# Optimization experiments

Hardware: AMD Instinct MI355X
Metric: run time of the kernel (lower is better)

Reference implementation:

```python
import jax, jax.numpy as jnp
import numpy as np

D_MODEL = 1024
NUM_HEADS = 16
HEAD_DIM = D_MODEL // NUM_HEADS


def setup_inputs() -> dict:
    key = jax.random.key(0)
    kx, kq, kk, kv, ko = jax.random.split(key, 5)
    B, S = 2, 2048
    scale = 1.0 / np.sqrt(D_MODEL)
    return {
        "x": jax.random.normal(kx, (B, S, D_MODEL), dtype=jnp.float32),
        "W_q": jax.random.normal(kq, (D_MODEL, D_MODEL), dtype=jnp.float32) * scale,
        "W_k": jax.random.normal(kk, (D_MODEL, D_MODEL), dtype=jnp.float32) * scale,
        "W_v": jax.random.normal(kv, (D_MODEL, D_MODEL), dtype=jnp.float32) * scale,
        "W_o": jax.random.normal(ko, (D_MODEL, D_MODEL), dtype=jnp.float32) * scale,
        "causal": 1,
    }


def _attn(x, W_q, W_k, W_v, W_o, causal):
    B, S, D = x.shape
    H, Hd = NUM_HEADS, HEAD_DIM
    # projections: nn.Linear applies x @ W.T
    q = (x @ W_q.T).reshape(B, S, H, Hd)
    k = (x @ W_k.T).reshape(B, S, H, Hd)
    v = (x @ W_v.T).reshape(B, S, H, Hd)
    # scores: [B, H, S, S]
    scores = jnp.einsum("bqhd,bkhd->bhqk", q, k) / np.sqrt(Hd)
    if causal:
        mask = jnp.triu(jnp.ones((S, S), dtype=bool), k=1)
        scores = jnp.where(mask, -jnp.inf, scores)
    attn = jax.nn.softmax(scores, axis=-1)
    out = jnp.einsum("bhqk,bkhd->bqhd", attn, v).reshape(B, S, D)
    return out @ W_o.T


def reference(x, W_q, W_k, W_v, W_o, causal):
    return _attn(x, W_q, W_k, W_v, W_o, causal)
```

## Files before the change

### kernel.cpp

```cpp
#include <hip/hip_runtime.h>

typedef __attribute__((ext_vector_type(8))) short bf16x8;
typedef __attribute__((ext_vector_type(4))) float f32x4;
typedef __attribute__((ext_vector_type(4))) unsigned short u16x4;

#define MFMA16(a, b, c) __builtin_amdgcn_mfma_f32_16x16x32_bf16((a), (b), (c), 0, 0, 0)

static constexpr int D_MODEL = 1024;
static constexpr int SEQ = 2048;
static constexpr int NH = 16;
static constexpr int HD = 64;
static constexpr int LDA = 40;
static constexpr int MST = 136;
static constexpr float NEG_BIG = -1.0e30f;

__device__ __forceinline__ unsigned short f2bf(float f) {
  union { float f; unsigned int u; } v; v.f = f;
  unsigned int r = v.u + 0x7fffu + ((v.u >> 16) & 1u);
  return (unsigned short)(r >> 16);
}

__device__ __forceinline__ unsigned int cvtpk_bf16(float a, float b) {
  unsigned int r;
  asm("v_cvt_pk_bf16_f32 %0, %1, %2" : "=v"(r) : "v"(a), "v"(b));
  return r;
}

__device__ __forceinline__ bf16x8 ld8(const void* p, size_t eidx, int bf) {
  if (bf) return *(const bf16x8*)((const unsigned short*)p + eidx);
  const float* f = (const float*)p + eidx;
  f32x4 lo = *(const f32x4*)f;
  f32x4 hi = *(const f32x4*)(f + 4);
  bf16x8 r;
  r[0] = (short)f2bf(lo[0]); r[1] = (short)f2bf(lo[1]);
  r[2] = (short)f2bf(lo[2]); r[3] = (short)f2bf(lo[3]);
  r[4] = (short)f2bf(hi[0]); r[5] = (short)f2bf(hi[1]);
  r[6] = (short)f2bf(hi[2]); r[7] = (short)f2bf(hi[3]);
  return r;
}

__device__ __forceinline__ void async16(const unsigned short* g, unsigned short* l) {
  __builtin_amdgcn_global_load_lds(
      (const __attribute__((address_space(1))) void*)g,
      (__attribute__((address_space(3))) void*)l, 16, 0, 0);
}

__global__ __launch_bounds__(64) void detect_kernel(
    const unsigned short* __restrict__ xs, int* __restrict__ flag) {
  int lane = threadIdx.x;
  unsigned short s = xs[2 * lane];
  int e = (s >> 7) & 0xFF;
  bool hit = (e >= 117 && e <= 129);
  unsigned long long m = __ballot(hit);
  if (lane == 0) { flag[0] = (__popcll(m) >= 32) ? 1 : 0; flag[1] = 1; }
}

__global__ __launch_bounds__(256) void convert_kernel(
    const void* __restrict__ X,
    const void* __restrict__ W0, const void* __restrict__ W1,
    const void* __restrict__ W2, const void* __restrict__ W3,
    const int* __restrict__ flag,
    unsigned short* __restrict__ Xb, unsigned short* __restrict__ Wb)
{
  const int bf = *flag;
  const int ty = blockIdx.y;
  const void* src; unsigned short* dst; size_t n;
  if (ty == 0) { src = X; dst = Xb; n = (size_t)2 * SEQ * D_MODEL; }
  else {
    src = (ty == 1) ? W0 : (ty == 2) ? W1 : (ty == 3) ? W2 : W3;
    dst = Wb + (size_t)(ty - 1) * D_MODEL * D_MODEL;
    n = (size_t)D_MODEL * D_MODEL;
  }
  size_t i = ((size_t)blockIdx.x * 256 + threadIdx.x) * 8;
  if (i >= n) return;
  *(bf16x8*)(dst + i) = ld8(src, i, bf);
}

__device__ __forceinline__ void gemm_fast_core(
    const unsigned short* __restrict__ A, const unsigned short* __restrict__ B,
    int tm, int tn, unsigned short* smem, f32x4 acc[4][4])
{
  const int t = threadIdx.x;
  const int lane = t & 63;
  const int w = t >> 6;
  const int wm = (w >> 1) * 64, wn = (w & 1) * 64;
  const int quad = lane >> 4, l16 = lane & 15;
  const int srow = lane >> 3;
  const int scol = ((lane & 7) ^ srow) * 8;
  const int xa = l16 & 7;

#pragma unroll
  for (int mi = 0; mi < 4; ++mi)
#pragma unroll
    for (int ni = 0; ni < 4; ++ni)
      acc[mi][ni] = (f32x4){0.f, 0.f, 0.f, 0.f};

#pragma unroll
  for (int j = 0; j < 4; ++j) {
    const int row = w * 32 + j * 8;
    async16(A + (size_t)(tm + row + srow) * D_MODEL + scol, smem + row * 64);
    async16(B + (size_t)(tn + row + srow) * D_MODEL + scol,
            smem + 8192 + row * 64);
  }

  for (int kt = 0; kt < 16; ++kt) {
    const int co = (kt & 1) << 14;
    asm volatile("s_waitcnt vmcnt(0)" ::: "memory");
    __syncthreads();
    if (kt < 15) {
      const int no = ((kt & 1) ^ 1) << 14;
      const int k0 = (kt + 1) * 64;
#pragma unroll
      for (int j = 0; j < 4; ++j) {
        const int row = w * 32 + j * 8;
        async16(A + (size_t)(tm + row + srow) * D_MODEL + k0 + scol,
                smem + no + row * 64);
        async16(B + (size_t)(tn + row + srow) * D_MODEL + k0 + scol,
                smem + no + 8192 + row * 64);
      }
    }
    bf16x8 af[2][4], bfv[2][4];
#pragma unroll
    for (int ks = 0; ks < 2; ++ks) {
#pragma unroll
      for (int mi = 0; mi < 4; ++mi)
        af[ks][mi] = *(const bf16x8*)(smem + co + (wm + mi * 16 + l16) * 64 +
                                      ((ks * 4 + quad) ^ xa) * 8);
#pragma unroll
      for (int ni = 0; ni < 4; ++ni)
        bfv[ks][ni] = *(const bf16x8*)(smem + co + 8192 +
                                       (wn + ni * 16 + l16) * 64 +
                                       ((ks * 4 + quad) ^ xa) * 8);
    }
    __builtin_amdgcn_s_setprio(1);
#pragma unroll
    for (int ks = 0; ks < 2; ++ks)
#pragma unroll
      for (int mi = 0; mi < 4; ++mi)
#pragma unroll
        for (int ni = 0; ni < 4; ++ni)
          acc[mi][ni] = MFMA16(af[ks][mi], bfv[ks][ni], acc[mi][ni]);
    __builtin_amdgcn_s_setprio(0);
  }
}

__global__ __launch_bounds__(256) void qkv_fast_kernel(
    const unsigned short* __restrict__ X,
    const unsigned short* __restrict__ Wb,
    unsigned short* __restrict__ qd,
    unsigned short* __restrict__ kws,
    unsigned short* __restrict__ vws)
{
  __shared__ __align__(16) unsigned short smem[4 * 128 * 64];
  const int bid = blockIdx.x;
  const int xcd = bid & 7, s0 = bid >> 3;
  const int tmg = xcd >> 2, tng = xcd & 3;
  const int tm_local = s0 / 6, zt = s0 % 6;
  const int z = zt >> 1, tn_local = zt & 1;
  const int tm = (tmg * 16 + tm_local) * 128;
  const int tn = (tng * 2 + tn_local) * 128;
  const unsigned short* W = Wb + (size_t)z * D_MODEL * D_MODEL;
  f32x4 acc[4][4];
  gemm_fast_core(X, W, tm, tn, smem, acc);

  const int t = threadIdx.x;
  const int lane = t & 63, w = t >> 6;
  const int wm = (w >> 1) * 64, wn = (w & 1) * 64;
  const int quad = lane >> 4, l16 = lane & 15;

  if (z == 2) {
    const int b = tm >> 11;
    const int sb = tm & 2047;
#pragma unroll
    for (int ph = 0; ph < 2; ++ph) {
      __syncthreads();
      if ((w & 1) == ph) {
#pragma unroll
        for (int mi = 0; mi < 4; ++mi)
#pragma unroll
          for (int ni = 0; ni < 4; ++ni)
#pragma unroll
            for (int r = 0; r < 4; ++r) {
              int m_local = wm + mi * 16 + quad * 4 + r;
              int n_sub = ni * 16 + l16;
              smem[n_sub * MST + m_local] = f2bf(acc[mi][ni][r]);
            }
      }
      __syncthreads();
      const int row = t >> 2, c0 = (t & 3) * 32;
      const int n_g = tn + ph * 64 + row;
      const int h = n_g >> 6, d = n_g & 63;
      unsigned short* dst = vws + (((size_t)b * NH + h) * HD + d) * SEQ + sb + c0;
#pragma unroll
      for (int cc = 0; cc < 4; ++cc)
        *(bf16x8*)(dst + cc * 8) = *(const bf16x8*)(smem + row * MST + c0 + cc * 8);
    }
    return;
  }
#pragma unroll
  for (int mi = 0; mi < 4; ++mi)
#pragma unroll
    for (int ni = 0; ni < 4; ++ni)
#pragma unroll
      for (int r = 0; r < 4; ++r) {
        int m = tm + wm + mi * 16 + quad * 4 + r;
        int n = tn + wn + ni * 16 + l16;
        unsigned short bv = f2bf(acc[mi][ni][r]);
        if (z == 0) {
          qd[(size_t)m * D_MODEL + n] = bv;
        } else {
          int b = m >> 11, sg = m & 2047;
          int h = n >> 6, d = n & 63;
          kws[(((size_t)b * NH + h) * SEQ + sg) * HD + d] = bv;
        }
      }
}

__global__ __launch_bounds__(256) void oproj_fast_kernel(
    const unsigned short* __restrict__ AW,
    const unsigned short* __restrict__ Wo,
    float* __restrict__ tmp)
{
  __shared__ __align__(16) unsigned short smem[4 * 128 * 64];
  const int bid = blockIdx.x;
  const int xcd = bid & 7, s0 = bid >> 3;
  const int tmg = xcd >> 2, tng = xcd & 3;
  const int tm = (tmg * 16 + (s0 >> 1)) * 128;
  const int tn = (tng * 2 + (s0 & 1)) * 128;
  f32x4 acc[4][4];
  gemm_fast_core(AW, Wo, tm, tn, smem, acc);

  const int t = threadIdx.x;
  const int lane = t & 63, w = t >> 6;
  const int wm = (w >> 1) * 64, wn = (w & 1) * 64;
  const int quad = lane >> 4, l16 = lane & 15;
#pragma unroll
  for (int mi = 0; mi < 4; ++mi)
#pragma unroll
    for (int ni = 0; ni < 4; ++ni)
#pragma unroll
      for (int r = 0; r < 4; ++r) {
        int m = tm + wm + mi * 16 + quad * 4 + r;
        int n = tn + wn + ni * 16 + l16;
        tmp[(size_t)m * D_MODEL + n] = acc[mi][ni][r];
      }
}

__device__ __forceinline__ void gemm_tile_128x128(
    const void* __restrict__ A, const void* __restrict__ B, int bf,
    int tm, int tn, unsigned short* As, unsigned short* Bs, f32x4 acc[4][4])
{
  const int t = threadIdx.x;
  const int lane = t & 63;
  const int w = t >> 6;
  const int wm = (w >> 1) * 64, wn = (w & 1) * 64;
  const int quad = lane >> 4, l16 = lane & 15;
  const int r0 = t >> 2, kc = (t & 3) * 8;
  const int r1 = r0 + 64;

#pragma unroll
  for (int mi = 0; mi < 4; ++mi)
#pragma unroll
    for (int ni = 0; ni < 4; ++ni)
      acc[mi][ni] = (f32x4){0.f, 0.f, 0.f, 0.f};

  for (int k0 = 0; k0 < D_MODEL; k0 += 32) {
    bf16x8 a0 = ld8(A, (size_t)(tm + r0) * D_MODEL + k0 + kc, bf);
    bf16x8 a1 = ld8(A, (size_t)(tm + r1) * D_MODEL + k0 + kc, bf);
    bf16x8 b0 = ld8(B, (size_t)(tn + r0) * D_MODEL + k0 + kc, bf);
    bf16x8 b1 = ld8(B, (size_t)(tn + r1) * D_MODEL + k0 + kc, bf);
    __syncthreads();
    *(bf16x8*)(As + r0 * LDA + kc) = a0;
    *(bf16x8*)(As + r1 * LDA + kc) = a1;
    *(bf16x8*)(Bs + r0 * LDA + kc) = b0;
    *(bf16x8*)(Bs + r1 * LDA + kc) = b1;
    __syncthreads();
    bf16x8 af[4], bfv[4];
#pragma unroll
    for (int mi = 0; mi < 4; ++mi)
      af[mi] = *(const bf16x8*)(As + (wm + mi * 16 + l16) * LDA + quad * 8);
#pragma unroll
    for (int ni = 0; ni < 4; ++ni)
      bfv[ni] = *(const bf16x8*)(Bs + (wn + ni * 16 + l16) * LDA + quad * 8);
#pragma unroll
    for (int mi = 0; mi < 4; ++mi)
#pragma unroll
      for (int ni = 0; ni < 4; ++ni)
        acc[mi][ni] = MFMA16(af[mi], bfv[ni], acc[mi][ni]);
  }
}

__global__ __launch_bounds__(256) void qkv_kernel(
    const void* __restrict__ X,
    const void* __restrict__ Wq,
    const void* __restrict__ Wk,
    const void* __restrict__ Wv,
    const int* __restrict__ flag,
    unsigned short* __restrict__ qd,
    unsigned short* __restrict__ kws,
    unsigned short* __restrict__ vws)
{
  __shared__ __align__(16) unsigned short As[128 * LDA];
  __shared__ __align__(16) unsigned short Bs[128 * LDA];
  const int bf = *flag;
  const int z = blockIdx.z;
  const void* W = (z == 0) ? Wq : ((z == 1) ? Wk : Wv);
  const int tm = blockIdx.y * 128, tn = blockIdx.x * 128;
  f32x4 acc[4][4];
  gemm_tile_128x128(X, W, bf, tm, tn, As, Bs, acc);

  const int t = threadIdx.x;
  const int lane = t & 63, w = t >> 6;
  const int wm = (w >> 1) * 64, wn = (w & 1) * 64;
  const int quad = lane >> 4, l16 = lane & 15;
#pragma unroll
  for (int mi = 0; mi < 4; ++mi)
#pragma unroll
    for (int ni = 0; ni < 4; ++ni)
#pragma unroll
      for (int r = 0; r < 4; ++r) {
        int m = tm + wm + mi * 16 + quad * 4 + r;
        int n = tn + wn + ni * 16 + l16;
        unsigned short bv = f2bf(acc[mi][ni][r]);
        if (z == 0) {
          qd[(size_t)m * D_MODEL + n] = bv;
        } else {
          int b = m >> 11, s = m & 2047;
          int h = n >> 6, d = n & 63;
          if (z == 1) kws[(((size_t)b * NH + h) * SEQ + s) * HD + d] = bv;
          else        vws[(((size_t)b * NH + h) * HD + d) * SEQ + s] = bv;
        }
      }
}

__global__ __launch_bounds__(256) void oproj_kernel(
    const unsigned short* __restrict__ AW,
    const void* __restrict__ Wo,
    const int* __restrict__ flag,
    float* __restrict__ tmp)
{
  __shared__ __align__(16) unsigned short As[128 * LDA];
  __shared__ __align__(16) unsigned short Bs[128 * LDA];
  const int bf = *flag;
  const int t = threadIdx.x;
  const int lane = t & 63;
  const int w = t >> 6;
  const int wm = (w >> 1) * 64, wn = (w & 1) * 64;
  const int quad = lane >> 4, l16 = lane & 15;
  const int r0 = t >> 2, kc = (t & 3) * 8;
  const int r1 = r0 + 64;
  const int tm = blockIdx.y * 128, tn = blockIdx.x * 128;
  f32x4 acc[4][4];
#pragma unroll
  for (int mi = 0; mi < 4; ++mi)
#pragma unroll
    for (int ni = 0; ni < 4; ++ni)
      acc[mi][ni] = (f32x4){0.f, 0.f, 0.f, 0.f};

  for (int k0 = 0; k0 < D_MODEL; k0 += 32) {
    bf16x8 a0 = *(const bf16x8*)(AW + (size_t)(tm + r0) * D_MODEL + k0 + kc);
    bf16x8 a1 = *(const bf16x8*)(AW + (size_t)(tm + r1) * D_MODEL + k0 + kc);
    bf16x8 b0 = ld8(Wo, (size_t)(tn + r0) * D_MODEL + k0 + kc, bf);
    bf16x8 b1 = ld8(Wo, (size_t)(tn + r1) * D_MODEL + k0 + kc, bf);
    __syncthreads();
    *(bf16x8*)(As + r0 * LDA + kc) = a0;
    *(bf16x8*)(As + r1 * LDA + kc) = a1;
    *(bf16x8*)(Bs + r0 * LDA + kc) = b0;
    *(bf16x8*)(Bs + r1 * LDA + kc) = b1;
    __syncthreads();
    bf16x8 af[4], bfv[4];
#pragma unroll
    for (int mi = 0; mi < 4; ++mi)
      af[mi] = *(const bf16x8*)(As + (wm + mi * 16 + l16) * LDA + quad * 8);
#pragma unroll
    for (int ni = 0; ni < 4; ++ni)
      bfv[ni] = *(const bf16x8*)(Bs + (wn + ni * 16 + l16) * LDA + quad * 8);
#pragma unroll
    for (int mi = 0; mi < 4; ++mi)
#pragma unroll
      for (int ni = 0; ni < 4; ++ni)
        acc[mi][ni] = MFMA16(af[mi], bfv[ni], acc[mi][ni]);
  }
#pragma unroll
  for (int mi = 0; mi < 4; ++mi)
#pragma unroll
    for (int ni = 0; ni < 4; ++ni)
#pragma unroll
      for (int r = 0; r < 4; ++r) {
        int m = tm + wm + mi * 16 + quad * 4 + r;
        int n = tn + wn + ni * 16 + l16;
        tmp[(size_t)m * D_MODEL + n] = acc[mi][ni][r];
      }
}

__global__ __launch_bounds__(128) void attn_kernel(
    unsigned short* __restrict__ Qd,
    const unsigned short* __restrict__ Kb,
    const unsigned short* __restrict__ Vt,
    const int* __restrict__ causal_p)
{
  __shared__ __align__(16) unsigned short Ks[2][64 * 64];
  __shared__ __align__(16) unsigned short Vs[2][64 * 64];
  const int bid = blockIdx.x;
  const int xcd = bid & 7, slot = bid >> 3;
  const int q = slot >> 5;
  const int r = slot & 31;
  const int gg = (q & 1) ? (31 - r) : r;
  const int bh = xcd * 4 + q;
  const int b = bh >> 4, h = bh & 15;
  const int t = threadIdx.x, lane = t & 63, w = t >> 6;
  const int quad = lane >> 4, l16 = lane & 15;
  const int causal = *causal_p;
  unsigned short* qh = Qd + (size_t)b * SEQ * D_MODEL + h * HD;
  const unsigned short* kh = Kb + ((size_t)b * NH + h) * SEQ * HD;
  const unsigned short* vh = Vt + ((size_t)b * NH + h) * HD * SEQ;
  const float Cs = 0.125f * 1.4426950408889634f;
  const int srow = lane >> 3;
  const int gcol = ((lane & 7) ^ srow) * 8;
  const int xa = l16 & 7;
  const int ktend = causal ? (gg + 1) : (SEQ / 64);

  int kvp[4];
#pragma unroll
  for (int j2 = 0; j2 < 4; ++j2) {
    const int rp = w * 32 + j2 * 8 + srow;
    kvp[j2] = ((rp >> 4) & 1) * 32 + ((rp >> 2) & 3) * 8 + ((rp >> 5) & 1) * 4 + (rp & 3);
  }

  int q0[2];
  bf16x8 aq[2][2];
#pragma unroll
  for (int s = 0; s < 2; ++s) {
    q0[s] = gg * 64 + w * 32 + s * 16;
#pragma unroll
    for (int ch = 0; ch < 2; ++ch)
      aq[s][ch] = *(const bf16x8*)(qh + (size_t)(q0[s] + l16) * D_MODEL +
                                   ch * 32 + quad * 8);
  }

  f32x4 oaccT[2][4];
#pragma unroll
  for (int s = 0; s < 2; ++s)
#pragma unroll
    for (int db = 0; db < 4; ++db) oaccT[s][db] = (f32x4){0.f, 0.f, 0.f, 0.f};
  float lsum[2] = {0.f, 0.f};

#pragma unroll
  for (int j2 = 0; j2 < 4; ++j2) {
    const int row = w * 32 + j2 * 8;
    async16(kh + (size_t)kvp[j2] * HD + gcol, &Ks[0][row * 64]);
    async16(vh + (size_t)(row + srow) * SEQ + gcol, &Vs[0][row * 64]);
  }

  for (int kt = 0; kt < ktend; ++kt) {
    const int cur = kt & 1;
    asm volatile("s_waitcnt vmcnt(0)" ::: "memory");
    __syncthreads();
    if (kt + 1 < ktend) {
      const int nxt = cur ^ 1;
#pragma unroll
      for (int j2 = 0; j2 < 4; ++j2) {
        const int row = w * 32 + j2 * 8;
        async16(kh + (size_t)((kt + 1) * 64 + kvp[j2]) * HD + gcol,
                &Ks[nxt][row * 64]);
        async16(vh + (size_t)(row + srow) * SEQ + (kt + 1) * 64 + gcol,
                &Vs[nxt][row * 64]);
      }
    }

    bf16x8 kfr[4][2], vfr[4][2];
#pragma unroll
    for (int cb = 0; cb < 4; ++cb)
#pragma unroll
      for (int hf = 0; hf < 2; ++hf) {
        kfr[cb][hf] = *(const bf16x8*)(&Ks[cur][(cb * 16 + l16) * 64 +
                                                ((hf * 4 + quad) ^ xa) * 8]);
        vfr[cb][hf] = *(const bf16x8*)(&Vs[cur][(cb * 16 + l16) * 64 +
                                                ((hf * 4 + quad) ^ xa) * 8]);
      }
#pragma unroll
    for (int s = 0; s < 2; ++s) {
      f32x4 sc[4];
      __builtin_amdgcn_s_setprio(1);
#pragma unroll
      for (int cb = 0; cb < 4; ++cb) {
        sc[cb] = (f32x4){0.f, 0.f, 0.f, 0.f};
        sc[cb] = MFMA16(kfr[cb][0], aq[s][0], sc[cb]);
        sc[cb] = MFMA16(kfr[cb][1], aq[s][1], sc[cb]);
      }
      __builtin_amdgcn_s_setprio(0);
      if (causal && kt == gg) {
        int qq = q0[s] + l16;
#pragma unroll
        for (int cb = 0; cb < 4; ++cb)
#pragma unroll
          for (int rr = 0; rr < 4; ++rr)
            if (kt * 64 + (cb & 1) * 32 + quad * 8 + (cb >> 1) * 4 + rr > qq)
              sc[cb][rr] = NEG_BIG;
      }
      float ls = 0.f;
#pragma unroll
      for (int cb = 0; cb < 4; ++cb)
#pragma unroll
        for (int rr = 0; rr < 4; ++rr) {
          float p = __builtin_amdgcn_exp2f(sc[cb][rr] * Cs);
          ls += p;
          sc[cb][rr] = p;
        }
      lsum[s] += ls;
      bf16x8 bp[2];
#pragma unroll
      for (int hf = 0; hf < 2; ++hf) {
        union { unsigned int w4[4]; bf16x8 v; } u;
        u.w4[0] = cvtpk_bf16(sc[hf][0], sc[hf][1]);
        u.w4[1] = cvtpk_bf16(sc[hf][2], sc[hf][3]);
        u.w4[2] = cvtpk_bf16(sc[2 + hf][0], sc[2 + hf][1]);
        u.w4[3] = cvtpk_bf16(sc[2 + hf][2], sc[2 + hf][3]);
        bp[hf] = u.v;
      }
      __builtin_amdgcn_s_setprio(1);
#pragma unroll
      for (int db = 0; db < 4; ++db) {
        oaccT[s][db] = MFMA16(vfr[db][0], bp[0], oaccT[s][db]);
        oaccT[s][db] = MFMA16(vfr[db][1], bp[1], oaccT[s][db]);
      }
      __builtin_amdgcn_s_setprio(0);
    }
  }
#pragma unroll
  for (int s = 0; s < 2; ++s) {
    float l = lsum[s];
    l += __shfl_xor(l, 16, 64);
    l += __shfl_xor(l, 32, 64);
    float inv = 1.0f / l;
#pragma unroll
    for (int db = 0; db < 4; ++db) {
      u16x4 o;
#pragma unroll
      for (int rr = 0; rr < 4; ++rr) o[rr] = f2bf(oaccT[s][db][rr] * inv);
      *(u16x4*)(qh + (size_t)(q0[s] + l16) * D_MODEL + db * 16 + quad * 4) = o;
    }
  }
}

__global__ __launch_bounds__(256) void final_kernel(
    const float* __restrict__ tmp, void* __restrict__ out,
    const int* __restrict__ flag)
{
  const int bf = *flag;
  size_t i = ((size_t)blockIdx.x * 256 + threadIdx.x) * 8;
  f32x4 lo = *(const f32x4*)(tmp + i);
  f32x4 hi = *(const f32x4*)(tmp + i + 4);
  if (bf) {
    bf16x8 r;
    r[0] = (short)f2bf(lo[0]); r[1] = (short)f2bf(lo[1]);
    r[2] = (short)f2bf(lo[2]); r[3] = (short)f2bf(lo[3]);
    r[4] = (short)f2bf(hi[0]); r[5] = (short)f2bf(hi[1]);
    r[6] = (short)f2bf(hi[2]); r[7] = (short)f2bf(hi[3]);
    *(bf16x8*)((unsigned short*)out + i) = r;
  } else {
    *(f32x4*)((float*)out + i) = lo;
    *(f32x4*)((float*)out + i + 4) = hi;
  }
}

extern "C" void kernel_launch(void* const* d_in, const int* in_sizes, int n_in,
                              void* d_out, int out_size, void* d_ws, size_t ws_size,
                              hipStream_t stream) {
  const void* X  = d_in[0];
  const void* Wq = d_in[1];
  const void* Wk = d_in[2];
  const void* Wv = d_in[3];
  const void* Wo = d_in[4];
  const int* causal = (const int*)d_in[5];

  const size_t NE = (size_t)2 * SEQ * D_MODEL;
  const size_t WE = (size_t)D_MODEL * D_MODEL;
  int* flag0 = (int*)d_ws;
  int* flag1 = flag0 + 1;
  unsigned short* kws = (unsigned short*)((char*)d_ws + 64);
  unsigned short* vws = kws + NE;
  float* tmp = (float*)kws;
  unsigned short* Wb = vws + NE;
  unsigned short* qd = (unsigned short*)d_out;
  unsigned short* Xb = qd + NE;

  const bool big = ws_size >= (size_t)64 + 24ull * 1024 * 1024;

  hipLaunchKernelGGL(detect_kernel, dim3(1), dim3(64), 0, stream,
                     (const unsigned short*)X, flag0);
  if (big) {
    hipLaunchKernelGGL(convert_kernel, dim3(2048, 5), dim3(256), 0, stream,
                       X, Wq, Wk, Wv, Wo, flag0, Xb, Wb);
    hipLaunchKernelGGL(qkv_fast_kernel, dim3(768), dim3(256), 0, stream,
                       Xb, Wb, qd, kws, vws);
    hipLaunchKernelGGL(attn_kernel, dim3(1024), dim3(128), 0, stream,
                       qd, kws, vws, causal);
    hipLaunchKernelGGL(oproj_fast_kernel, dim3(256), dim3(256), 0, stream,
                       qd, Wb + 3 * WE, tmp);
  } else {
    hipLaunchKernelGGL(qkv_kernel, dim3(8, 32, 3), dim3(256), 0, stream,
                       X, Wq, Wk, Wv, flag0, qd, kws, vws);
    hipLaunchKernelGGL(attn_kernel, dim3(1024), dim3(128), 0, stream,
                       qd, kws, vws, causal);
    hipLaunchKernelGGL(oproj_kernel, dim3(8, 32), dim3(256), 0, stream,
                       qd, Wo, flag0, tmp);
  }
  hipLaunchKernelGGL(final_kernel, dim3(2048), dim3(256), 0, stream,
                     tmp, d_out, flag0);
}
```

Measured before the change: 202.1 us.

## Pair complementary causal query tiles per attention block with triple-buffered KV

Measured after the change: 200.1 us. About the same (-1.0%).

```diff
diff --git a/kernel.cpp b/kernel.cpp
--- a/kernel.cpp
+++ b/kernel.cpp
@@ -393,24 +393,91 @@
       }
 }
 
-__global__ __launch_bounds__(128) void attn_kernel(
+__device__ __forceinline__ void attn_item(
+    const unsigned short* __restrict__ Ksb, const unsigned short* __restrict__ Vsb,
+    const bf16x8 (&aq)[2][2], f32x4 (&oaccT)[2][4], float (&lsum)[2],
+    int kt, int diag, int q0base, int l16, int quad, int xa, float Cs)
+{
+  bf16x8 kfr[4][2], vfr[4][2];
+#pragma unroll
+  for (int cb = 0; cb < 4; ++cb)
+#pragma unroll
+    for (int hf = 0; hf < 2; ++hf) {
+      kfr[cb][hf] = *(const bf16x8*)(Ksb + (cb * 16 + l16) * 64 +
+                                     ((hf * 4 + quad) ^ xa) * 8);
+      vfr[cb][hf] = *(const bf16x8*)(Vsb + (cb * 16 + l16) * 64 +
+                                     ((hf * 4 + quad) ^ xa) * 8);
+    }
+#pragma unroll
+  for (int s = 0; s < 2; ++s) {
+    f32x4 sc[4];
+    __builtin_amdgcn_s_setprio(1);
+#pragma unroll
+    for (int cb = 0; cb < 4; ++cb) {
+      sc[cb] = (f32x4){0.f, 0.f, 0.f, 0.f};
+      sc[cb] = MFMA16(kfr[cb][0], aq[s][0], sc[cb]);
+      sc[cb] = MFMA16(kfr[cb][1], aq[s][1], sc[cb]);
+    }
+    __builtin_amdgcn_s_setprio(0);
+    if (diag) {
+      int qq = q0base + s * 16 + l16;
+#pragma unroll
+      for (int cb = 0; cb < 4; ++cb)
+#pragma unroll
+        for (int rr = 0; rr < 4; ++rr)
+          if (kt * 64 + (cb & 1) * 32 + quad * 8 + (cb >> 1) * 4 + rr > qq)
+            sc[cb][rr] = NEG_BIG;
+    }
+    float ls = 0.f;
+#pragma unroll
+    for (int cb = 0; cb < 4; ++cb)
+#pragma unroll
+      for (int rr = 0; rr < 4; ++rr) {
+        float pv = __builtin_amdgcn_exp2f(sc[cb][rr] * Cs);
+        ls += pv;
+        sc[cb][rr] = pv;
+      }
+    lsum[s] += ls;
+    bf16x8 bp[2];
+#pragma unroll
+    for (int hf = 0; hf < 2; ++hf) {
+      union { unsigned int w4[4]; bf16x8 v; } u;
+      u.w4[0] = cvtpk_bf16(sc[hf][0], sc[hf][1]);
+      u.w4[1] = cvtpk_bf16(sc[hf][2], sc[hf][3]);
+      u.w4[2] = cvtpk_bf16(sc[2 + hf][0], sc[2 + hf][1]);
+      u.w4[3] = cvtpk_bf16(sc[2 + hf][2], sc[2 + hf][3]);
+      bp[hf] = u.v;
+    }
+    __builtin_amdgcn_s_setprio(1);
+#pragma unroll
+    for (int db = 0; db < 4; ++db) {
+      oaccT[s][db] = MFMA16(vfr[db][0], bp[0], oaccT[s][db]);
+      oaccT[s][db] = MFMA16(vfr[db][1], bp[1], oaccT[s][db]);
+    }
+    __builtin_amdgcn_s_setprio(0);
+  }
+}
+
+__global__ __launch_bounds__(128, 1) void attn_kernel(
     unsigned short* __restrict__ Qd,
     const unsigned short* __restrict__ Kb,
     const unsigned short* __restrict__ Vt,
     const int* __restrict__ causal_p)
 {
-  __shared__ __align__(16) unsigned short Ks[2][64 * 64];
-  __shared__ __align__(16) unsigned short Vs[2][64 * 64];
+  __shared__ __align__(16) unsigned short Ks[3][64 * 64];
+  __shared__ __align__(16) unsigned short Vs[3][64 * 64];
   const int bid = blockIdx.x;
   const int xcd = bid & 7, slot = bid >> 3;
-  const int q = slot >> 5;
-  const int r = slot & 31;
-  const int gg = (q & 1) ? (31 - r) : r;
-  const int bh = xcd * 4 + q;
+  const int bhl = slot >> 4, p = slot & 15;
+  const int bh = xcd * 4 + bhl;
   const int b = bh >> 4, h = bh & 15;
   const int t = threadIdx.x, lane = t & 63, w = t >> 6;
   const int quad = lane >> 4, l16 = lane & 15;
   const int causal = *causal_p;
+  const int tA = causal ? (31 - p) : (2 * p);
+  const int tB = causal ? p : (2 * p + 1);
+  const int ktA = causal ? (32 - p) : 32;
+  const int ITEMS = causal ? 33 : 64;
   unsigned short* qh = Qd + (size_t)b * SEQ * D_MODEL + h * HD;
   const unsigned short* kh = Kb + ((size_t)b * NH + h) * SEQ * HD;
   const unsigned short* vh = Vt + ((size_t)b * NH + h) * HD * SEQ;
@@ -418,7 +485,6 @@
   const int srow = lane >> 3;
   const int gcol = ((lane & 7) ^ srow) * 8;
   const int xa = l16 & 7;
-  const int ktend = causal ? (gg + 1) : (SEQ / 64);
 
   int kvp[4];
 #pragma unroll
@@ -427,109 +493,61 @@
     kvp[j2] = ((rp >> 4) & 1) * 32 + ((rp >> 2) & 3) * 8 + ((rp >> 5) & 1) * 4 + (rp & 3);
   }
 
-  int q0[2];
-  bf16x8 aq[2][2];
+  const int qA = tA * 64 + w * 32, qB = tB * 64 + w * 32;
+  bf16x8 aqA[2][2], aqB[2][2];
+#pragma unroll
+  for (int s = 0; s < 2; ++s)
+#pragma unroll
+    for (int ch = 0; ch < 2; ++ch) {
+      aqA[s][ch] = *(const bf16x8*)(qh + (size_t)(qA + s * 16 + l16) * D_MODEL +
+                                    ch * 32 + quad * 8);
+      aqB[s][ch] = *(const bf16x8*)(qh + (size_t)(qB + s * 16 + l16) * D_MODEL +
+                                    ch * 32 + quad * 8);
+    }
+
+  f32x4 oaccA[2][4], oaccB[2][4];
+#pragma unroll
+  for (int s = 0; s < 2; ++s)
+#pragma unroll
+    for (int db = 0; db < 4; ++db) {
+      oaccA[s][db] = (f32x4){0.f, 0.f, 0.f, 0.f};
+      oaccB[s][db] = (f32x4){0.f, 0.f, 0.f, 0.f};
+    }
+  float lsumA[2] = {0.f, 0.f}, lsumB[2] = {0.f, 0.f};
+
+  auto stage = [&](int f, int buf) {
+    const int kt = (f < ktA) ? f : (f - ktA);
+#pragma unroll
+    for (int j2 = 0; j2 < 4; ++j2) {
+      const int row = w * 32 + j2 * 8;
+      async16(kh + (size_t)(kt * 64 + kvp[j2]) * HD + gcol, &Ks[buf][row * 64]);
+      async16(vh + (size_t)(row + srow) * SEQ + kt * 64 + gcol, &Vs[buf][row * 64]);
+    }
+  };
+
+  stage(0, 0);
+  stage(1, 1);
+
+  int cur = 0, nb = 2;
+  for (int f = 0; f < ITEMS; ++f) {
+    if (f + 1 < ITEMS) asm volatile("s_waitcnt vmcnt(8)" ::: "memory");
+    else               asm volatile("s_waitcnt vmcnt(0)" ::: "memory");
+    __builtin_amdgcn_s_barrier();
+    __builtin_amdgcn_sched_barrier(0);
+    if (f + 2 < ITEMS) stage(f + 2, nb);
+    if (f < ktA)
+      attn_item(&Ks[cur][0], &Vs[cur][0], aqA, oaccA, lsumA,
+                f, causal && (f == ktA - 1), qA, l16, quad, xa, Cs);
+    else
+      attn_item(&Ks[cur][0], &Vs[cur][0], aqB, oaccB, lsumB,
+                f - ktA, causal && (f == ITEMS - 1), qB, l16, quad, xa, Cs);
+    cur = (cur == 2) ? 0 : cur + 1;
+    nb = (nb == 2) ? 0 : nb + 1;
+  }
+
 #pragma unroll
   for (int s = 0; s < 2; ++s) {
-    q0[s] = gg * 64 + w * 32 + s * 16;
-#pragma unroll
-    for (int ch = 0; ch < 2; ++ch)
-      aq[s][ch] = *(const bf16x8*)(qh + (size_t)(q0[s] + l16) * D_MODEL +
-                                   ch * 32 + quad * 8);
-  }
-
-  f32x4 oaccT[2][4];
-#pragma unroll
-  for (int s = 0; s < 2; ++s)
-#pragma unroll
-    for (int db = 0; db < 4; ++db) oaccT[s][db] = (f32x4){0.f, 0.f, 0.f, 0.f};
-  float lsum[2] = {0.f, 0.f};
-
-#pragma unroll
-  for (int j2 = 0; j2 < 4; ++j2) {
-    const int row = w * 32 + j2 * 8;
-    async16(kh + (size_t)kvp[j2] * HD + gcol, &Ks[0][row * 64]);
-    async16(vh + (size_t)(row + srow) * SEQ + gcol, &Vs[0][row * 64]);
-  }
-
-  for (int kt = 0; kt < ktend; ++kt) {
-    const int cur = kt & 1;
-    asm volatile("s_waitcnt vmcnt(0)" ::: "memory");
-    __syncthreads();
-    if (kt + 1 < ktend) {
-      const int nxt = cur ^ 1;
-#pragma unroll
-      for (int j2 = 0; j2 < 4; ++j2) {
-        const int row = w * 32 + j2 * 8;
-        async16(kh + (size_t)((kt + 1) * 64 + kvp[j2]) * HD + gcol,
-                &Ks[nxt][row * 64]);
-        async16(vh + (size_t)(row + srow) * SEQ + (kt + 1) * 64 + gcol,
-                &Vs[nxt][row * 64]);
-      }
-    }
-
-    bf16x8 kfr[4][2], vfr[4][2];
-#pragma unroll
-    for (int cb = 0; cb < 4; ++cb)
-#pragma unroll
-      for (int hf = 0; hf < 2; ++hf) {
-        kfr[cb][hf] = *(const bf16x8*)(&Ks[cur][(cb * 16 + l16) * 64 +
-                                                ((hf * 4 + quad) ^ xa) * 8]);
-        vfr[cb][hf] = *(const bf16x8*)(&Vs[cur][(cb * 16 + l16) * 64 +
-                                                ((hf * 4 + quad) ^ xa) * 8]);
-      }
-#pragma unroll
-    for (int s = 0; s < 2; ++s) {
-      f32x4 sc[4];
-      __builtin_amdgcn_s_setprio(1);
-#pragma unroll
-      for (int cb = 0; cb < 4; ++cb) {
-        sc[cb] = (f32x4){0.f, 0.f, 0.f, 0.f};
-        sc[cb] = MFMA16(kfr[cb][0], aq[s][0], sc[cb]);
-        sc[cb] = MFMA16(kfr[cb][1], aq[s][1], sc[cb]);
-      }
-      __builtin_amdgcn_s_setprio(0);
-      if (causal && kt == gg) {
-        int qq = q0[s] + l16;
-#pragma unroll
-        for (int cb = 0; cb < 4; ++cb)
-#pragma unroll
-          for (int rr = 0; rr < 4; ++rr)
-            if (kt * 64 + (cb & 1) * 32 + quad * 8 + (cb >> 1) * 4 + rr > qq)
-              sc[cb][rr] = NEG_BIG;
-      }
-      float ls = 0.f;
-#pragma unroll
-      for (int cb = 0; cb < 4; ++cb)
-#pragma unroll
-        for (int rr = 0; rr < 4; ++rr) {
-          float p = __builtin_amdgcn_exp2f(sc[cb][rr] * Cs);
-          ls += p;
-          sc[cb][rr] = p;
-        }
-      lsum[s] += ls;
-      bf16x8 bp[2];
-#pragma unroll
-      for (int hf = 0; hf < 2; ++hf) {
-        union { unsigned int w4[4]; bf16x8 v; } u;
-        u.w4[0] = cvtpk_bf16(sc[hf][0], sc[hf][1]);
-        u.w4[1] = cvtpk_bf16(sc[hf][2], sc[hf][3]);
-        u.w4[2] = cvtpk_bf16(sc[2 + hf][0], sc[2 + hf][1]);
-        u.w4[3] = cvtpk_bf16(sc[2 + hf][2], sc[2 + hf][3]);
-        bp[hf] = u.v;
-      }
-      __builtin_amdgcn_s_setprio(1);
-#pragma unroll
-      for (int db = 0; db < 4; ++db) {
-        oaccT[s][db] = MFMA16(vfr[db][0], bp[0], oaccT[s][db]);
-        oaccT[s][db] = MFMA16(vfr[db][1], bp[1], oaccT[s][db]);
-      }
-      __builtin_amdgcn_s_setprio(0);
-    }
-  }
-#pragma unroll
-  for (int s = 0; s < 2; ++s) {
-    float l = lsum[s];
+    float l = lsumA[s];
     l += __shfl_xor(l, 16, 64);
     l += __shfl_xor(l, 32, 64);
     float inv = 1.0f / l;
@@ -537,8 +555,22 @@
     for (int db = 0; db < 4; ++db) {
       u16x4 o;
 #pragma unroll
-      for (int rr = 0; rr < 4; ++rr) o[rr] = f2bf(oaccT[s][db][rr] * inv);
-      *(u16x4*)(qh + (size_t)(q0[s] + l16) * D_MODEL + db * 16 + quad * 4) = o;
+      for (int rr = 0; rr < 4; ++rr) o[rr] = f2bf(oaccA[s][db][rr] * inv);
+      *(u16x4*)(qh + (size_t)(qA + s * 16 + l16) * D_MODEL + db * 16 + quad * 4) = o;
+    }
+  }
+#pragma unroll
+  for (int s = 0; s < 2; ++s) {
+    float l = lsumB[s];
+    l += __shfl_xor(l, 16, 64);
+    l += __shfl_xor(l, 32, 64);
+    float inv = 1.0f / l;
+#pragma unroll
+    for (int db = 0; db < 4; ++db) {
+      u16x4 o;
+#pragma unroll
+      for (int rr = 0; rr < 4; ++rr) o[rr] = f2bf(oaccB[s][db][rr] * inv);
+      *(u16x4*)(qh + (size_t)(qB + s * 16 + l16) * D_MODEL + db * 16 + quad * 4) = o;
     }
   }
 }
@@ -577,7 +609,6 @@
   const size_t NE = (size_t)2 * SEQ * D_MODEL;
   const size_t WE = (size_t)D_MODEL * D_MODEL;
   int* flag0 = (int*)d_ws;
-  int* flag1 = flag0 + 1;
   unsigned short* kws = (unsigned short*)((char*)d_ws + 64);
   unsigned short* vws = kws + NE;
   float* tmp = (float*)kws;
@@ -594,14 +625,14 @@
                        X, Wq, Wk, Wv, Wo, flag0, Xb, Wb);
     hipLaunchKernelGGL(qkv_fast_kernel, dim3(768), dim3(256), 0, stream,
                        Xb, Wb, qd, kws, vws);
-    hipLaunchKernelGGL(attn_kernel, dim3(1024), dim3(128), 0, stream,
+    hipLaunchKernelGGL(attn_kernel, dim3(512), dim3(128), 0, stream,
                        qd, kws, vws, causal);
     hipLaunchKernelGGL(oproj_fast_kernel, dim3(256), dim3(256), 0, stream,
                        qd, Wb + 3 * WE, tmp);
   } else {
     hipLaunchKernelGGL(qkv_kernel, dim3(8, 32, 3), dim3(256), 0, stream,
                        X, Wq, Wk, Wv, flag0, qd, kws, vws);
-    hipLaunchKernelGGL(attn_kernel, dim3(1024), dim3(128), 0, stream,
+    hipLaunchKernelGGL(attn_kernel, dim3(512), dim3(128), 0, stream,
                        qd, kws, vws, causal);
     hipLaunchKernelGGL(oproj_kernel, dim3(8, 32), dim3(256), 0, stream,
                        qd, Wo, flag0, tmp);
```
